# Kernel optimization log

Measured on AMD Instinct MI355X. Metric: run time of the kernel, lower is better.

## Reference

```python
import jax, jax.numpy as jnp
import numpy as np

N_HEAD = 16
N_EMBED = 1024

def setup_inputs() -> dict:
    key = jax.random.key(0)
    ks = jax.random.split(key, 5)
    s = 0.02
    return {
        "x": jax.random.normal(ks[0], (2, 2048, N_EMBED), dtype=jnp.float32),
        "W_attn": jax.random.normal(ks[1], (N_EMBED, 3 * N_EMBED), dtype=jnp.float32) * s,
        "b_attn": jax.random.normal(ks[2], (3 * N_EMBED,), dtype=jnp.float32) * s,
        "W_proj": jax.random.normal(ks[3], (N_EMBED, N_EMBED), dtype=jnp.float32) * s,
        "b_proj": jax.random.normal(ks[4], (N_EMBED,), dtype=jnp.float32) * s,
    }

def reference(x, W_attn, b_attn, W_proj, b_proj):
    B, T, C = x.shape
    H = N_HEAD
    hs = C // H
    qkv = x @ W_attn + b_attn                      # [B,T,3C]
    q, k, v = jnp.split(qkv, 3, axis=-1)
    # [B,T,C] -> [B,H,T,hs]
    q = q.reshape(B, T, H, hs).transpose(0, 2, 1, 3)
    k = k.reshape(B, T, H, hs).transpose(0, 2, 1, 3)
    v = v.reshape(B, T, H, hs).transpose(0, 2, 1, 3)
    scale = 1.0 / np.sqrt(hs).astype(np.float32)
    att = jnp.einsum('bhqd,bhkd->bhqk', q, k) * scale  # [B,H,T,T]
    causal = jnp.tril(jnp.ones((T, T), dtype=bool))
    att = jnp.where(causal, att, jnp.finfo(att.dtype).min)
    att = jax.nn.softmax(att, axis=-1)
    y = jnp.einsum('bhqk,bhkd->bhqd', att, v)      # [B,H,T,hs]
    y = y.transpose(0, 2, 1, 3).reshape(B, T, C)
    return y @ W_proj + b_proj
```

## Files before the change

kernel.cpp:

```cpp
#include <hip/hip_runtime.h>
#include <stdint.h>

#define T_SEQ 2048
#define CDIM 1024
#define NHEAD 16
#define HS 64

typedef __bf16 bf16x8 __attribute__((ext_vector_type(8)));
typedef float f32x4 __attribute__((ext_vector_type(4)));
typedef float f32x16 __attribute__((ext_vector_type(16)));

__device__ __forceinline__ unsigned short f2bf(float f) {
  union { float f; unsigned u; } c; c.f = f;
  unsigned r = c.u + 0x7FFFu + ((c.u >> 16) & 1u);
  return (unsigned short)(r >> 16);
}

__device__ __forceinline__ void gload_lds16(const void* g, void* l) {
  __builtin_amdgcn_global_load_lds((__attribute__((address_space(1))) void*)(g),
                                   (__attribute__((address_space(3))) void*)(l),
                                   16, 0, 0);
}

__device__ __forceinline__ float xhalf_other(float x, int hi) {
  union { float f; unsigned u; } c; c.f = x;
  auto r = __builtin_amdgcn_permlane32_swap(c.u, c.u, false, false);
  union { unsigned u; float f; } lo_, hi_;
  lo_.u = (unsigned)r[0]; hi_.u = (unsigned)r[1];
  return hi ? lo_.f : hi_.f;
}

__global__ __launch_bounds__(256) void k_cvt_x(const float* __restrict__ x,
                                               unsigned short* __restrict__ xb) {
  int i = blockIdx.x * 256 + threadIdx.x;
  float4 f = reinterpret_cast<const float4*>(x)[i];
  ushort4 u;
  u.x = f2bf(f.x); u.y = f2bf(f.y); u.z = f2bf(f.z); u.w = f2bf(f.w);
  reinterpret_cast<ushort4*>(xb)[i] = u;
}

__global__ __launch_bounds__(256) void k_transpose(const float* __restrict__ W,
                                                   unsigned short* __restrict__ Wt,
                                                   int K, int N) {
  __shared__ float tile[32][33];
  int n0 = blockIdx.x * 32, k0 = blockIdx.y * 32;
  int c = threadIdx.x & 31, r0 = threadIdx.x >> 5;
#pragma unroll
  for (int r = r0; r < 32; r += 8) tile[r][c] = W[(size_t)(k0 + r) * N + n0 + c];
  __syncthreads();
#pragma unroll
  for (int r = r0; r < 32; r += 8) Wt[(size_t)(n0 + r) * K + k0 + c] = f2bf(tile[c][r]);
}

template <int MODE, int KD>
__global__ __launch_bounds__(256) void k_gemm(const unsigned short* __restrict__ A,
                                              const unsigned short* __restrict__ Bt,
                                              const float* __restrict__ bias,
                                              float* __restrict__ outF,
                                              unsigned short* __restrict__ qb,
                                              unsigned short* __restrict__ kb,
                                              unsigned short* __restrict__ vb) {
  __shared__ __align__(16) unsigned short Al[128 * 32];
  __shared__ __align__(16) unsigned short Bl[128 * 32];
  const int tid = threadIdx.x;
  const int wave = tid >> 6, lane = tid & 63;
  const int m0 = blockIdx.x * 128, n0 = blockIdx.y * 128;
  const int wr = (wave >> 1) * 64, wc = (wave & 1) * 64;
  const int srow = tid >> 2, scol = (tid & 3) * 8;
  const int ka = (lane >> 4) * 8;
  f32x4 acc[4][4];
#pragma unroll
  for (int m = 0; m < 4; ++m)
#pragma unroll
    for (int n = 0; n < 4; ++n) acc[m][n] = f32x4{0.f, 0.f, 0.f, 0.f};

  for (int k0 = 0; k0 < KD; k0 += 32) {
#pragma unroll
    for (int r = 0; r < 2; ++r) {
      gload_lds16(A + (size_t)(m0 + r * 64 + srow) * KD + k0 + scol,
                  (char*)Al + r * 4096 + wave * 1024);
      gload_lds16(Bt + (size_t)(n0 + r * 64 + srow) * KD + k0 + scol,
                  (char*)Bl + r * 4096 + wave * 1024);
    }
    __syncthreads();
    bf16x8 af[4], bfr[4];
#pragma unroll
    for (int m = 0; m < 4; ++m)
      af[m] = *(const bf16x8*)&Al[(wr + m * 16 + (lane & 15)) * 32 + ka];
#pragma unroll
    for (int n = 0; n < 4; ++n)
      bfr[n] = *(const bf16x8*)&Bl[(wc + n * 16 + (lane & 15)) * 32 + ka];
#pragma unroll
    for (int m = 0; m < 4; ++m)
#pragma unroll
      for (int n = 0; n < 4; ++n)
        acc[m][n] = __builtin_amdgcn_mfma_f32_16x16x32_bf16(af[m], bfr[n], acc[m][n], 0, 0, 0);
    __syncthreads();
  }

#pragma unroll
  for (int m = 0; m < 4; ++m)
#pragma unroll
    for (int n = 0; n < 4; ++n)
#pragma unroll
      for (int j = 0; j < 4; ++j) {
        int row = m0 + wr + m * 16 + (lane >> 4) * 4 + j;
        int col = n0 + wc + n * 16 + (lane & 15);
        float v = acc[m][n][j] + bias[col];
        if (MODE == 1) {
          outF[(size_t)row * CDIM + col] = v;
        } else {
          int which = col >> 10;
          int h = (col >> 6) & 15;
          int d = col & 63;
          int b = row >> 11, t = row & (T_SEQ - 1);
          int bh = b * NHEAD + h;
          unsigned short bv = f2bf(which == 1 ? v * 0.18033688f : v);
          size_t tb = ((size_t)bh * 32 + (t >> 6)) * 4096;
          if (which == 2) {
            vb[tb + (d >> 5) * 2048 + ((t >> 4) & 3) * 512 + (d & 31) * 16 +
               ((t >> 3) & 1) * 8 + (t & 7)] = bv;
          } else {
            size_t a = tb + ((t >> 5) & 1) * 2048 + (d >> 4) * 512 + (t & 31) * 16 +
                       ((d >> 3) & 1) * 8 + (d & 7);
            if (which == 0) qb[a] = bv; else kb[a] = bv;
          }
        }
      }
}

#define MOSTR 67
__global__ __launch_bounds__(192) void k_attn(const unsigned short* __restrict__ qb,
                                              const unsigned short* __restrict__ kb,
                                              const unsigned short* __restrict__ vb,
                                              unsigned short* __restrict__ yb) {
  __shared__ float Mo[3 * 32 * MOSTR];
  __shared__ float Lml[3][2][32];
  const int rid = blockIdx.x;
  const int xcd = rid & 7, i = rid >> 3;
  const int bh = xcd * 4 + (i & 3);
  const int p = i >> 2;
  const int wave = threadIdx.x >> 6;
  const int lane = threadIdx.x & 63;
  const int l31 = lane & 31, hi = lane >> 5;
  const unsigned short* qh = qb + (size_t)bh * T_SEQ * HS;
  const unsigned short* kh = kb + (size_t)bh * T_SEQ * HS;
  const unsigned short* vh = vb + (size_t)bh * T_SEQ * HS;
  const int b = bh >> 4, h = bh & 15;
  const int lbase = l31 * 16 + hi * 8;

  for (int grp = 0; grp < 2; ++grp) {
    const int g = grp ? p : 63 - p;
    const int q0 = g * 32;
    const int nkt = (q0 >> 6) + 1;

    const size_t qbase = (size_t)(g >> 1) * 4096 + (size_t)(g & 1) * 2048;
    bf16x8 qf[4];
#pragma unroll
    for (int dd = 0; dd < 4; ++dd)
      qf[dd] = *(const bf16x8*)&qh[qbase + dd * 512 + lbase];

    f32x16 o2[2];
#pragma unroll
    for (int db = 0; db < 2; ++db)
#pragma unroll
      for (int e = 0; e < 16; ++e) o2[db][e] = 0.f;
    float Mx = -INFINITY, Ls = 0.f;

    bf16x8 kf[2][4];
#pragma unroll
    for (int kbk = 0; kbk < 2; ++kbk)
#pragma unroll
      for (int dd = 0; dd < 4; ++dd)
        kf[kbk][dd] = *(const bf16x8*)&kh[(size_t)wave * 4096 + kbk * 2048 + dd * 512 + lbase];
    f32x16 s[2];
#pragma unroll
    for (int kbk = 0; kbk < 2; ++kbk) {
      f32x16 z;
#pragma unroll
      for (int e = 0; e < 16; ++e) z[e] = 0.f;
#pragma unroll
      for (int dd = 0; dd < 4; ++dd)
        z = __builtin_amdgcn_mfma_f32_32x32x16_bf16(kf[kbk][dd], qf[dd], z, 0, 0, 0);
      s[kbk] = z;
    }

    for (int kt = wave; kt < nkt; kt += 3) {
      const int kvb = kt * 64;
      const bool more = (kt + 3 < nkt);

      if (more) {
#pragma unroll
        for (int kbk = 0; kbk < 2; ++kbk)
#pragma unroll
          for (int dd = 0; dd < 4; ++dd)
            kf[kbk][dd] = *(const bf16x8*)&kh[(size_t)(kt + 3) * 4096 + kbk * 2048 + dd * 512 + lbase];
      }
      bf16x8 vf[2][4];
#pragma unroll
      for (int db = 0; db < 2; ++db)
#pragma unroll
        for (int t16 = 0; t16 < 4; ++t16)
          vf[db][t16] = *(const bf16x8*)&vh[(size_t)kt * 4096 + db * 2048 + t16 * 512 + lbase];

      if (kvb + 63 > q0) {
        const int qg = q0 + l31;
#pragma unroll
        for (int kbk = 0; kbk < 2; ++kbk)
#pragma unroll
          for (int r = 0; r < 16; ++r) {
            const int key = kvb + kbk * 32 + (r & 3) + 8 * (r >> 2) + 4 * hi;
            if (key > qg) s[kbk][r] = -3.0e38f;
          }
      }

      f32x16 tm;
#pragma unroll
      for (int e = 0; e < 16; ++e) tm[e] = fmaxf(s[0][e], s[1][e]);
      float m8[8];
#pragma unroll
      for (int e = 0; e < 8; ++e) m8[e] = fmaxf(tm[e], tm[e + 8]);
      float m4a = fmaxf(m8[0], m8[4]), m4b = fmaxf(m8[1], m8[5]);
      float m4c = fmaxf(m8[2], m8[6]), m4d = fmaxf(m8[3], m8[7]);
      float mx = fmaxf(fmaxf(m4a, m4b), fmaxf(m4c, m4d));
      mx = fmaxf(mx, xhalf_other(mx, hi));

      if (!__all(mx <= Mx + 8.f)) {
        const float newM = fmaxf(Mx, mx);
        const float alpha = __builtin_exp2f(Mx - newM);
        Mx = newM;
        Ls *= alpha;
#pragma unroll
        for (int db = 0; db < 2; ++db)
#pragma unroll
          for (int e = 0; e < 16; ++e) o2[db][e] *= alpha;
      }

#pragma unroll
      for (int kbk = 0; kbk < 2; ++kbk)
#pragma unroll
        for (int r = 0; r < 16; ++r) s[kbk][r] = __builtin_exp2f(s[kbk][r] - Mx);
      f32x16 ts;
#pragma unroll
      for (int e = 0; e < 16; ++e) ts[e] = s[0][e] + s[1][e];
      float s8[8];
#pragma unroll
      for (int e = 0; e < 8; ++e) s8[e] = ts[e] + ts[e + 8];
      float rs = ((s8[0] + s8[1]) + (s8[2] + s8[3])) + ((s8[4] + s8[5]) + (s8[6] + s8[7]));
      rs += xhalf_other(rs, hi);
      Ls += rs;

      unsigned W0[2][4], W1[2][4];
#pragma unroll
      for (int kbk = 0; kbk < 2; ++kbk)
#pragma unroll
        for (int rg = 0; rg < 4; ++rg) {
          unsigned lo, hiw;
          asm("v_cvt_pk_bf16_f32 %0, %1, %2" : "=v"(lo) : "v"(s[kbk][4 * rg + 0]), "v"(s[kbk][4 * rg + 1]));
          asm("v_cvt_pk_bf16_f32 %0, %1, %2" : "=v"(hiw) : "v"(s[kbk][4 * rg + 2]), "v"(s[kbk][4 * rg + 3]));
          W0[kbk][rg] = lo; W1[kbk][rg] = hiw;
        }

      bf16x8 pf[4];
#pragma unroll
      for (int t16 = 0; t16 < 4; ++t16) {
        const int kbk = t16 >> 1, par = t16 & 1;
        unsigned a0 = W0[kbk][2 * par], b0 = W0[kbk][2 * par + 1];
        unsigned a1 = W1[kbk][2 * par], b1 = W1[kbk][2 * par + 1];
        auto r0 = __builtin_amdgcn_permlane32_swap(a0, b0, false, false);
        auto r1 = __builtin_amdgcn_permlane32_swap(a1, b1, false, false);
        union { unsigned u[4]; bf16x8 v; } cv;
        cv.u[0] = (unsigned)r0[0]; cv.u[1] = (unsigned)r1[0];
        cv.u[2] = (unsigned)r0[1]; cv.u[3] = (unsigned)r1[1];
        pf[t16] = cv.v;
      }

#pragma unroll
      for (int db = 0; db < 2; ++db)
#pragma unroll
        for (int t16 = 0; t16 < 4; ++t16)
          o2[db] = __builtin_amdgcn_mfma_f32_32x32x16_bf16(vf[db][t16], pf[t16], o2[db], 0, 0, 0);

      if (more) {
#pragma unroll
        for (int kbk = 0; kbk < 2; ++kbk) {
          f32x16 z;
#pragma unroll
          for (int e = 0; e < 16; ++e) z[e] = 0.f;
#pragma unroll
          for (int dd = 0; dd < 4; ++dd)
            z = __builtin_amdgcn_mfma_f32_32x32x16_bf16(kf[kbk][dd], qf[dd], z, 0, 0, 0);
          s[kbk] = z;
        }
      }
    }

    if (hi == 0) {
      Lml[wave][0][l31] = Mx;
      Lml[wave][1][l31] = Ls;
    }
#pragma unroll
    for (int db = 0; db < 2; ++db)
#pragma unroll
      for (int r = 0; r < 16; ++r)
        Mo[wave * 32 * MOSTR + l31 * MOSTR + db * 32 + (r & 3) + 8 * (r >> 2) + 4 * hi] = o2[db][r];
    __syncthreads();

    for (int c = threadIdx.x; c < 256; c += 192) {
      const int rl = c >> 3, c0 = (c & 7) * 8;
      const float m0 = Lml[0][0][rl], m1 = Lml[1][0][rl], m2 = Lml[2][0][rl];
      const float l0 = Lml[0][1][rl], l1 = Lml[1][1][rl], l2 = Lml[2][1][rl];
      const float M = fmaxf(fmaxf(m0, m1), m2);
      const float a0 = __builtin_exp2f(m0 - M);
      const float a1 = __builtin_exp2f(m1 - M);
      const float a2 = __builtin_exp2f(m2 - M);
      const float inv = 1.0f / (a0 * l0 + a1 * l1 + a2 * l2);
      const float* O0 = &Mo[rl * MOSTR + c0];
      const float* O1 = O0 + 32 * MOSTR;
      const float* O2 = O0 + 64 * MOSTR;
      unsigned pk[4];
#pragma unroll
      for (int e = 0; e < 4; ++e) {
        float va = (a0 * O0[2 * e] + a1 * O1[2 * e] + a2 * O2[2 * e]) * inv;
        float vb2 = (a0 * O0[2 * e + 1] + a1 * O1[2 * e + 1] + a2 * O2[2 * e + 1]) * inv;
        pk[e] = (unsigned)f2bf(va) | ((unsigned)f2bf(vb2) << 16);
      }
      uint4 u; u.x = pk[0]; u.y = pk[1]; u.z = pk[2]; u.w = pk[3];
      *(uint4*)&yb[(size_t)(b * T_SEQ + q0 + rl) * CDIM + h * 64 + c0] = u;
    }
    __syncthreads();
  }
}

extern "C" void kernel_launch(void* const* d_in, const int* in_sizes, int n_in,
                              void* d_out, int out_size, void* d_ws, size_t ws_size,
                              hipStream_t stream) {
  (void)in_sizes; (void)n_in; (void)out_size; (void)ws_size;
  const float* x      = (const float*)d_in[0];
  const float* W_attn = (const float*)d_in[1];
  const float* b_attn = (const float*)d_in[2];
  const float* W_proj = (const float*)d_in[3];
  const float* b_proj = (const float*)d_in[4];
  float* out = (float*)d_out;
  char* ws = (char*)d_ws;

  unsigned short* xb  = (unsigned short*)(ws);
  unsigned short* Wta = (unsigned short*)(ws + 8388608);
  unsigned short* Wtp = (unsigned short*)(ws + 14680064);
  unsigned short* qbf = (unsigned short*)(ws + 16777216);
  unsigned short* kbf = (unsigned short*)(ws + 25165824);
  unsigned short* vbf = (unsigned short*)(ws + 33554432);
  unsigned short* ybf = (unsigned short*)(ws + 41943040);

  k_cvt_x<<<4096, 256, 0, stream>>>(x, xb);
  k_transpose<<<dim3(96, 32), 256, 0, stream>>>(W_attn, Wta, 1024, 3072);
  k_transpose<<<dim3(32, 32), 256, 0, stream>>>(W_proj, Wtp, 1024, 1024);
  k_gemm<0, 1024><<<dim3(32, 24), 256, 0, stream>>>(xb, Wta, b_attn, nullptr, qbf, kbf, vbf);
  k_attn<<<1024, 192, 0, stream>>>(qbf, kbf, vbf, ybf);
  k_gemm<1, 1024><<<dim3(32, 8), 256, 0, stream>>>(ybf, Wtp, b_proj, out, nullptr, nullptr, nullptr);
}
```

Measured before the change: 130.5 us.

## Merge prep kernels, use four attention waves, shrink projection GEMM tile

Folds the x conversion and both weight transposes into one prep launch so fewer kernels are launched. The attention kernel goes from three to four waves per block, which splits the key tiles four ways and merges four partial softmax states. The output projection GEMM moves to a 64x128 tile, giving 512 blocks instead of 256 so more CUs are busy. The costs are more LDS per attention block and less data reuse per block in the projection GEMM.

```diff
diff --git a/kernel.cpp b/kernel.cpp
--- a/kernel.cpp
+++ b/kernel.cpp
@@ -30,36 +30,44 @@
   return hi ? lo_.f : hi_.f;
 }
 
-__global__ __launch_bounds__(256) void k_cvt_x(const float* __restrict__ x,
-                                               unsigned short* __restrict__ xb) {
-  int i = blockIdx.x * 256 + threadIdx.x;
-  float4 f = reinterpret_cast<const float4*>(x)[i];
-  ushort4 u;
-  u.x = f2bf(f.x); u.y = f2bf(f.y); u.z = f2bf(f.z); u.w = f2bf(f.w);
-  reinterpret_cast<ushort4*>(xb)[i] = u;
-}
-
-__global__ __launch_bounds__(256) void k_transpose(const float* __restrict__ W,
-                                                   unsigned short* __restrict__ Wt,
-                                                   int K, int N) {
+__global__ __launch_bounds__(256) void k_prep(const float* __restrict__ x,
+                                              unsigned short* __restrict__ xb,
+                                              const float* __restrict__ Wa,
+                                              unsigned short* __restrict__ Wta,
+                                              const float* __restrict__ Wp,
+                                              unsigned short* __restrict__ Wtp) {
   __shared__ float tile[32][33];
-  int n0 = blockIdx.x * 32, k0 = blockIdx.y * 32;
+  const int bid = blockIdx.x;
+  if (bid < 4096) {
+    int i = bid * 256 + threadIdx.x;
+    float4 f = reinterpret_cast<const float4*>(x)[i];
+    ushort4 u;
+    u.x = f2bf(f.x); u.y = f2bf(f.y); u.z = f2bf(f.z); u.w = f2bf(f.w);
+    reinterpret_cast<ushort4*>(xb)[i] = u;
+    return;
+  }
+  const float* W; unsigned short* Wt; int N, n0, k0;
+  if (bid < 7168) {
+    int b2 = bid - 4096; W = Wa; Wt = Wta; N = 3072;
+    n0 = (b2 % 96) * 32; k0 = (b2 / 96) * 32;
+  } else {
+    int b2 = bid - 7168; W = Wp; Wt = Wtp; N = 1024;
+    n0 = (b2 & 31) * 32; k0 = (b2 >> 5) * 32;
+  }
   int c = threadIdx.x & 31, r0 = threadIdx.x >> 5;
 #pragma unroll
   for (int r = r0; r < 32; r += 8) tile[r][c] = W[(size_t)(k0 + r) * N + n0 + c];
   __syncthreads();
 #pragma unroll
-  for (int r = r0; r < 32; r += 8) Wt[(size_t)(n0 + r) * K + k0 + c] = f2bf(tile[c][r]);
-}
-
-template <int MODE, int KD>
-__global__ __launch_bounds__(256) void k_gemm(const unsigned short* __restrict__ A,
-                                              const unsigned short* __restrict__ Bt,
-                                              const float* __restrict__ bias,
-                                              float* __restrict__ outF,
-                                              unsigned short* __restrict__ qb,
-                                              unsigned short* __restrict__ kb,
-                                              unsigned short* __restrict__ vb) {
+  for (int r = r0; r < 32; r += 8) Wt[(size_t)(n0 + r) * 1024 + k0 + c] = f2bf(tile[c][r]);
+}
+
+__global__ __launch_bounds__(256) void k_gemm1(const unsigned short* __restrict__ A,
+                                               const unsigned short* __restrict__ Bt,
+                                               const float* __restrict__ bias,
+                                               unsigned short* __restrict__ qb,
+                                               unsigned short* __restrict__ kb,
+                                               unsigned short* __restrict__ vb) {
   __shared__ __align__(16) unsigned short Al[128 * 32];
   __shared__ __align__(16) unsigned short Bl[128 * 32];
   const int tid = threadIdx.x;
@@ -74,12 +82,12 @@
 #pragma unroll
     for (int n = 0; n < 4; ++n) acc[m][n] = f32x4{0.f, 0.f, 0.f, 0.f};
 
-  for (int k0 = 0; k0 < KD; k0 += 32) {
+  for (int k0 = 0; k0 < 1024; k0 += 32) {
 #pragma unroll
     for (int r = 0; r < 2; ++r) {
-      gload_lds16(A + (size_t)(m0 + r * 64 + srow) * KD + k0 + scol,
+      gload_lds16(A + (size_t)(m0 + r * 64 + srow) * 1024 + k0 + scol,
                   (char*)Al + r * 4096 + wave * 1024);
-      gload_lds16(Bt + (size_t)(n0 + r * 64 + srow) * KD + k0 + scol,
+      gload_lds16(Bt + (size_t)(n0 + r * 64 + srow) * 1024 + k0 + scol,
                   (char*)Bl + r * 4096 + wave * 1024);
     }
     __syncthreads();
@@ -107,35 +115,83 @@
         int row = m0 + wr + m * 16 + (lane >> 4) * 4 + j;
         int col = n0 + wc + n * 16 + (lane & 15);
         float v = acc[m][n][j] + bias[col];
-        if (MODE == 1) {
-          outF[(size_t)row * CDIM + col] = v;
+        int which = col >> 10;
+        int h = (col >> 6) & 15;
+        int d = col & 63;
+        int b = row >> 11, t = row & (T_SEQ - 1);
+        int bh = b * NHEAD + h;
+        unsigned short bv = f2bf(which == 1 ? v * 0.18033688f : v);
+        size_t tb = ((size_t)bh * 32 + (t >> 6)) * 4096;
+        if (which == 2) {
+          vb[tb + (d >> 5) * 2048 + ((t >> 4) & 3) * 512 + (d & 31) * 16 +
+             ((t >> 3) & 1) * 8 + (t & 7)] = bv;
         } else {
-          int which = col >> 10;
-          int h = (col >> 6) & 15;
-          int d = col & 63;
-          int b = row >> 11, t = row & (T_SEQ - 1);
-          int bh = b * NHEAD + h;
-          unsigned short bv = f2bf(which == 1 ? v * 0.18033688f : v);
-          size_t tb = ((size_t)bh * 32 + (t >> 6)) * 4096;
-          if (which == 2) {
-            vb[tb + (d >> 5) * 2048 + ((t >> 4) & 3) * 512 + (d & 31) * 16 +
-               ((t >> 3) & 1) * 8 + (t & 7)] = bv;
-          } else {
-            size_t a = tb + ((t >> 5) & 1) * 2048 + (d >> 4) * 512 + (t & 31) * 16 +
-                       ((d >> 3) & 1) * 8 + (d & 7);
-            if (which == 0) qb[a] = bv; else kb[a] = bv;
-          }
+          size_t a = tb + ((t >> 5) & 1) * 2048 + (d >> 4) * 512 + (t & 31) * 16 +
+                     ((d >> 3) & 1) * 8 + (d & 7);
+          if (which == 0) qb[a] = bv; else kb[a] = bv;
         }
       }
 }
 
+__global__ __launch_bounds__(256) void k_gemm2(const unsigned short* __restrict__ A,
+                                               const unsigned short* __restrict__ Bt,
+                                               const float* __restrict__ bias,
+                                               float* __restrict__ outF) {
+  __shared__ __align__(16) unsigned short Al[64 * 32];
+  __shared__ __align__(16) unsigned short Bl[128 * 32];
+  const int tid = threadIdx.x;
+  const int wave = tid >> 6, lane = tid & 63;
+  const int m0 = blockIdx.x * 64, n0 = blockIdx.y * 128;
+  const int wr = (wave >> 1) * 32, wc = (wave & 1) * 64;
+  const int srow = tid >> 2, scol = (tid & 3) * 8;
+  const int ka = (lane >> 4) * 8;
+  f32x4 acc[2][4];
+#pragma unroll
+  for (int m = 0; m < 2; ++m)
+#pragma unroll
+    for (int n = 0; n < 4; ++n) acc[m][n] = f32x4{0.f, 0.f, 0.f, 0.f};
+
+  for (int k0 = 0; k0 < 1024; k0 += 32) {
+    gload_lds16(A + (size_t)(m0 + srow) * 1024 + k0 + scol, (char*)Al + wave * 1024);
+#pragma unroll
+    for (int r = 0; r < 2; ++r)
+      gload_lds16(Bt + (size_t)(n0 + r * 64 + srow) * 1024 + k0 + scol,
+                  (char*)Bl + r * 4096 + wave * 1024);
+    __syncthreads();
+    bf16x8 af[2], bfr[4];
+#pragma unroll
+    for (int m = 0; m < 2; ++m)
+      af[m] = *(const bf16x8*)&Al[(wr + m * 16 + (lane & 15)) * 32 + ka];
+#pragma unroll
+    for (int n = 0; n < 4; ++n)
+      bfr[n] = *(const bf16x8*)&Bl[(wc + n * 16 + (lane & 15)) * 32 + ka];
+#pragma unroll
+    for (int m = 0; m < 2; ++m)
+#pragma unroll
+      for (int n = 0; n < 4; ++n)
+        acc[m][n] = __builtin_amdgcn_mfma_f32_16x16x32_bf16(af[m], bfr[n], acc[m][n], 0, 0, 0);
+    __syncthreads();
+  }
+
+#pragma unroll
+  for (int m = 0; m < 2; ++m)
+#pragma unroll
+    for (int n = 0; n < 4; ++n)
+#pragma unroll
+      for (int j = 0; j < 4; ++j) {
+        int row = m0 + wr + m * 16 + (lane >> 4) * 4 + j;
+        int col = n0 + wc + n * 16 + (lane & 15);
+        outF[(size_t)row * CDIM + col] = acc[m][n][j] + bias[col];
+      }
+}
+
 #define MOSTR 67
-__global__ __launch_bounds__(192) void k_attn(const unsigned short* __restrict__ qb,
+__global__ __launch_bounds__(256) void k_attn(const unsigned short* __restrict__ qb,
                                               const unsigned short* __restrict__ kb,
                                               const unsigned short* __restrict__ vb,
                                               unsigned short* __restrict__ yb) {
-  __shared__ float Mo[3 * 32 * MOSTR];
-  __shared__ float Lml[3][2][32];
+  __shared__ float Mo[4 * 32 * MOSTR];
+  __shared__ float Lml[4][2][32];
   const int rid = blockIdx.x;
   const int xcd = rid & 7, i = rid >> 3;
   const int bh = xcd * 4 + (i & 3);
@@ -185,16 +241,16 @@
       s[kbk] = z;
     }
 
-    for (int kt = wave; kt < nkt; kt += 3) {
+    for (int kt = wave; kt < nkt; kt += 4) {
       const int kvb = kt * 64;
-      const bool more = (kt + 3 < nkt);
+      const bool more = (kt + 4 < nkt);
 
       if (more) {
 #pragma unroll
         for (int kbk = 0; kbk < 2; ++kbk)
 #pragma unroll
           for (int dd = 0; dd < 4; ++dd)
-            kf[kbk][dd] = *(const bf16x8*)&kh[(size_t)(kt + 3) * 4096 + kbk * 2048 + dd * 512 + lbase];
+            kf[kbk][dd] = *(const bf16x8*)&kh[(size_t)(kt + 4) * 4096 + kbk * 2048 + dd * 512 + lbase];
       }
       bf16x8 vf[2][4];
 #pragma unroll
@@ -306,23 +362,26 @@
         Mo[wave * 32 * MOSTR + l31 * MOSTR + db * 32 + (r & 3) + 8 * (r >> 2) + 4 * hi] = o2[db][r];
     __syncthreads();
 
-    for (int c = threadIdx.x; c < 256; c += 192) {
+    {
+      const int c = threadIdx.x;
       const int rl = c >> 3, c0 = (c & 7) * 8;
-      const float m0 = Lml[0][0][rl], m1 = Lml[1][0][rl], m2 = Lml[2][0][rl];
-      const float l0 = Lml[0][1][rl], l1 = Lml[1][1][rl], l2 = Lml[2][1][rl];
-      const float M = fmaxf(fmaxf(m0, m1), m2);
+      const float m0 = Lml[0][0][rl], m1 = Lml[1][0][rl], m2 = Lml[2][0][rl], m3 = Lml[3][0][rl];
+      const float l0 = Lml[0][1][rl], l1 = Lml[1][1][rl], l2 = Lml[2][1][rl], l3 = Lml[3][1][rl];
+      const float M = fmaxf(fmaxf(m0, m1), fmaxf(m2, m3));
       const float a0 = __builtin_exp2f(m0 - M);
       const float a1 = __builtin_exp2f(m1 - M);
       const float a2 = __builtin_exp2f(m2 - M);
-      const float inv = 1.0f / (a0 * l0 + a1 * l1 + a2 * l2);
+      const float a3 = __builtin_exp2f(m3 - M);
+      const float inv = 1.0f / (a0 * l0 + a1 * l1 + a2 * l2 + a3 * l3);
       const float* O0 = &Mo[rl * MOSTR + c0];
       const float* O1 = O0 + 32 * MOSTR;
       const float* O2 = O0 + 64 * MOSTR;
+      const float* O3 = O0 + 96 * MOSTR;
       unsigned pk[4];
 #pragma unroll
       for (int e = 0; e < 4; ++e) {
-        float va = (a0 * O0[2 * e] + a1 * O1[2 * e] + a2 * O2[2 * e]) * inv;
-        float vb2 = (a0 * O0[2 * e + 1] + a1 * O1[2 * e + 1] + a2 * O2[2 * e + 1]) * inv;
+        float va = (a0 * O0[2 * e] + a1 * O1[2 * e] + a2 * O2[2 * e] + a3 * O3[2 * e]) * inv;
+        float vb2 = (a0 * O0[2 * e + 1] + a1 * O1[2 * e + 1] + a2 * O2[2 * e + 1] + a3 * O3[2 * e + 1]) * inv;
         pk[e] = (unsigned)f2bf(va) | ((unsigned)f2bf(vb2) << 16);
       }
       uint4 u; u.x = pk[0]; u.y = pk[1]; u.z = pk[2]; u.w = pk[3];
@@ -352,10 +411,8 @@
   unsigned short* vbf = (unsigned short*)(ws + 33554432);
   unsigned short* ybf = (unsigned short*)(ws + 41943040);
 
-  k_cvt_x<<<4096, 256, 0, stream>>>(x, xb);
-  k_transpose<<<dim3(96, 32), 256, 0, stream>>>(W_attn, Wta, 1024, 3072);
-  k_transpose<<<dim3(32, 32), 256, 0, stream>>>(W_proj, Wtp, 1024, 1024);
-  k_gemm<0, 1024><<<dim3(32, 24), 256, 0, stream>>>(xb, Wta, b_attn, nullptr, qbf, kbf, vbf);
-  k_attn<<<1024, 192, 0, stream>>>(qbf, kbf, vbf, ybf);
-  k_gemm<1, 1024><<<dim3(32, 8), 256, 0, stream>>>(ybf, Wtp, b_proj, out, nullptr, nullptr, nullptr);
-}
+  k_prep<<<8192, 256, 0, stream>>>(x, xb, W_attn, Wta, W_proj, Wtp);
+  k_gemm1<<<dim3(32, 24), 256, 0, stream>>>(xb, Wta, b_attn, qbf, kbf, vbf);
+  k_attn<<<1024, 256, 0, stream>>>(qbf, kbf, vbf, ybf);
+  k_gemm2<<<dim3(64, 8), 256, 0, stream>>>(ybf, Wtp, b_proj, out);
+}
```

New measurement: 114.1 us. 12.6% less time.
